# Kernel optimization log

Measured on AMD Instinct MI355X. Metric: run time of the kernel, lower is better.

Reference implementation:

```python
import jax, jax.numpy as jnp
import numpy as np

B, NV, NQ, NA = 128, 100, 14, 10
V_DIM, Q_DIM, A_DIM = 2048, 1024, 1024
H_DIM, RANK, HD, G = 512, 32, 16, 2  # HD = H_DIM // RANK, G = glimpse


def setup_inputs() -> dict:
    key = jax.random.key(0)
    ks = jax.random.split(key, 16)
    s = 0.05
    return {
        "v": jax.random.normal(ks[0], (B, NV, V_DIM), jnp.float32),
        "q": jax.random.normal(ks[1], (B, NQ, Q_DIM), jnp.float32),
        "a": jax.random.normal(ks[2], (B, NA, A_DIM), jnp.float32),
        # tucker projections (FCNet = Linear + ReLU; dropout identity at eval)
        "Wv": jax.random.normal(ks[3], (H_DIM, V_DIM), jnp.float32) * s,
        "bv": jnp.zeros((H_DIM,), jnp.float32),
        "Wq": jax.random.normal(ks[4], (H_DIM, Q_DIM), jnp.float32) * s,
        "bq": jnp.zeros((H_DIM,), jnp.float32),
        "Wa": jax.random.normal(ks[5], (H_DIM, A_DIM), jnp.float32) * s,
        "ba": jnp.zeros((H_DIM,), jnp.float32),
        # rank-wise projection nets, stacked over rank: [rank, HD, H_DIM]
        "Wvr": jax.random.normal(ks[6], (RANK, HD, H_DIM), jnp.float32) * s,
        "bvr": jnp.zeros((RANK, HD), jnp.float32),
        "Wqr": jax.random.normal(ks[7], (RANK, HD, H_DIM), jnp.float32) * s,
        "bqr": jnp.zeros((RANK, HD), jnp.float32),
        "War": jax.random.normal(ks[8], (RANK, HD, H_DIM), jnp.float32) * s,
        "bar": jnp.zeros((RANK, HD), jnp.float32),
        # Tucker core T_g with h_out squeezed: [rank, hv, hq, ha, glimpse]
        "T": jax.random.normal(ks[9], (RANK, HD, HD, HD, G), jnp.float32),
    }


def reference(v, q, a, Wv, bv, Wq, bq, Wa, ba, Wvr, bvr, Wqr, bqr, War, bar, T):
    relu = jax.nn.relu
    # modality tucker projections: [B, N, H_DIM]
    vt = relu(jnp.einsum('bnd,hd->bnh', v, Wv) + bv)
    qt = relu(jnp.einsum('bnd,hd->bnh', q, Wq) + bq)
    at = relu(jnp.einsum('bnd,hd->bnh', a, Wa) + ba)
    # rank-wise FCNets, batched over rank: [B, rank, N, HD]
    v_ = relu(jnp.einsum('bnh,rch->brnc', vt, Wvr) + bvr[None, :, None, :])
    q_ = relu(jnp.einsum('bnh,rch->brnc', qt, Wqr) + bqr[None, :, None, :])
    a_ = relu(jnp.einsum('bnh,rch->brnc', at, War) + bar[None, :, None, :])
    # 6-way Tucker contraction, summed over rank: [B, NV, NQ, NA, G]
    f_emb = jnp.einsum('rijkg,bnvi,bnqj,bnak->bvqag', T, v_, q_, a_,
                       optimize=True)
    return f_emb
```

## Files before the change

kernel.cpp:

```cpp
#include <hip/hip_runtime.h>
#include <cstddef>
#include <cstdint>

#define B_    128
#define NV_   100
#define NQ_   14
#define NA_   10
#define HDIM  512
#define RANK_ 32
#define HD_   16
#define G_    2

typedef __bf16 bf16x8 __attribute__((ext_vector_type(8)));
typedef float  f32x4  __attribute__((ext_vector_type(4)));
union Frag { uint4 u; bf16x8 v; };

__device__ __forceinline__ unsigned int f2bf(float f) {
  unsigned int u = __float_as_uint(f);
  u = (u + 0x7FFFu + ((u >> 16) & 1u)) >> 16;
  return u & 0xFFFFu;
}

__device__ __forceinline__ void gload_lds16(const unsigned short* gp,
                                            unsigned short* dp) {
  __builtin_amdgcn_global_load_lds(
      (const __attribute__((address_space(1))) void*)gp,
      (__attribute__((address_space(3))) void*)dp, 16, 0, 0);
}

__global__ __launch_bounds__(256) void cvt_kernel(
    const float* __restrict__ s0, const float* __restrict__ s1,
    const float* __restrict__ s2, const float* __restrict__ s3,
    const float* __restrict__ s4, const float* __restrict__ s5,
    const float* __restrict__ s6, const float* __restrict__ s7,
    unsigned short* __restrict__ dst)
{
  const int pref[8] = {896, 1536, 2048, 2304, 2560, 2688, 2816, 2944};
  const float* srcs[8] = {s0, s1, s2, s3, s4, s5, s6, s7};
  const int blk = blockIdx.x;
  int seg = 0;
  #pragma unroll
  for (int i = 0; i < 7; ++i) if (blk >= pref[i]) seg = i + 1;
  const int base_chunk = seg ? pref[seg - 1] : 0;
  const size_t loc = (size_t)(blk - base_chunk) * 2048 + threadIdx.x * 8;
  const float* s = srcs[seg] + loc;
  float4 f0 = *(const float4*)s;
  float4 f1 = *(const float4*)(s + 4);
  ushort4 o0, o1;
  o0.x = f2bf(f0.x); o0.y = f2bf(f0.y); o0.z = f2bf(f0.z); o0.w = f2bf(f0.w);
  o1.x = f2bf(f1.x); o1.y = f2bf(f1.y); o1.z = f2bf(f1.z); o1.w = f2bf(f1.w);
  unsigned short* d = dst + (size_t)blk * 2048 + threadIdx.x * 8;
  *(ushort4*)d = o0;
  *(ushort4*)(d + 4) = o1;
}

__device__ __forceinline__ void stage_swz8(const unsigned short* __restrict__ src,
                                           int K, unsigned short* dst, int t)
{
  const int wb = t & 448;
  const int l = t & 63;
  #pragma unroll
  for (int i = 0; i < 2; ++i) {
    const int sb = i * 512 + wb;
    const int li = sb + l;
    const int row = li >> 3;
    const int p = li & 7;
    const int s = p ^ (row & 7);
    gload_lds16(src + (size_t)row * K + s * 8, dst + sb * 8);
  }
}

__device__ __forceinline__ void cvt_write(const float4 f[4], unsigned short* Abuf,
                                          int ar, int kq)
{
  unsigned short* base = Abuf + ar * 64;
  #pragma unroll
  for (int j = 0; j < 2; ++j) {
    uint4 p;
    p.x = f2bf(f[2*j].x)   | (f2bf(f[2*j].y)   << 16);
    p.y = f2bf(f[2*j].z)   | (f2bf(f[2*j].w)   << 16);
    p.z = f2bf(f[2*j+1].x) | (f2bf(f[2*j+1].y) << 16);
    p.w = f2bf(f[2*j+1].z) | (f2bf(f[2*j+1].w) << 16);
    const int s = (kq * 2 + j) ^ (ar & 7);
    *(uint4*)&base[s * 8] = p;
  }
}

__global__ __launch_bounds__(512, 4) void l1_gemm(
    const float* __restrict__ v,
    const unsigned short* __restrict__ qb, const unsigned short* __restrict__ ab,
    const unsigned short* __restrict__ Wvb, const unsigned short* __restrict__ Wqb,
    const unsigned short* __restrict__ Wab,
    const float* __restrict__ bv, const float* __restrict__ bq,
    const float* __restrict__ ba,
    unsigned short* __restrict__ vtb, unsigned short* __restrict__ qtb,
    unsigned short* __restrict__ atb)
{
  __shared__ __align__(16) unsigned short As[2][8192];
  __shared__ __align__(16) unsigned short Bs[2][8192];
  const int bx = blockIdx.x;
  int grp, gx, gy, K;
  const unsigned short *A16 = qb, *W;
  const float* bias;
  unsigned short* C;
  if (bx < 400) {
    grp = 0; const int xcd = bx & 7, j = bx >> 3; const int m = xcd * 50 + j;
    gy = m >> 2; gx = m & 3; W = Wvb; bias = bv; C = vtb; K = 2048;
  } else if (bx < 456) {
    grp = 1; const int lo = bx - 400; gy = lo >> 2; gx = lo & 3;
    A16 = qb; W = Wqb; bias = bq; C = qtb; K = 1024;
  } else {
    grp = 2; const int lo = bx - 456; gy = lo >> 2; gx = lo & 3;
    A16 = ab; W = Wab; bias = ba; C = atb; K = 1024;
  }
  const int nsteps = K >> 6;
  const int bm = gy * 128, bn = gx * 128;
  const int t = threadIdx.x;
  const int w = t >> 6, l = t & 63;
  const int wm = (w >> 2) * 64, wn = (w & 3) * 32;

  f32x4 acc[4][2];
  #pragma unroll
  for (int i = 0; i < 4; ++i)
    #pragma unroll
    for (int j = 0; j < 2; ++j) acc[i][j] = f32x4{0.f, 0.f, 0.f, 0.f};

  const int ar = t >> 2, kq = t & 3;
  const float* vrow = (grp == 0)
      ? v + (size_t)(bm + ar) * 2048 + kq * 16 : (const float*)nullptr;
  float4 R0[4], R1[4];

  stage_swz8(W + (size_t)bn * K, K, Bs[0], t);
  if (grp == 0) {
    #pragma unroll
    for (int i = 0; i < 4; ++i) R0[i] = ((const float4*)vrow)[i];
    #pragma unroll
    for (int i = 0; i < 4; ++i) R1[i] = ((const float4*)(vrow + 64))[i];
    cvt_write(R0, As[0], ar, kq);
  } else {
    stage_swz8(A16 + (size_t)bm * K, K, As[0], t);
  }
  __syncthreads();

  for (int step = 0; step < nsteps; ++step) {
    const int db = step & 1;
    const bool hn = (step + 1) < nsteps;
    if (hn) stage_swz8(W + (size_t)bn * K + (step + 1) * 64, K, Bs[db ^ 1], t);
    if (grp == 0) {
      if (step + 2 < nsteps) {
        const float* p = vrow + (step + 2) * 64;
        if (db == 0) {
          #pragma unroll
          for (int i = 0; i < 4; ++i) R0[i] = ((const float4*)p)[i];
        } else {
          #pragma unroll
          for (int i = 0; i < 4; ++i) R1[i] = ((const float4*)p)[i];
        }
      }
      if (hn) {
        if (db == 0) cvt_write(R1, As[1], ar, kq);
        else         cvt_write(R0, As[0], ar, kq);
      }
    } else if (hn) {
      stage_swz8(A16 + (size_t)bm * K + (step + 1) * 64, K, As[db ^ 1], t);
    }
    const unsigned short* Ad = As[db];
    const unsigned short* Bd = Bs[db];
    #pragma unroll
    for (int ks = 0; ks < 2; ++ks) {
      Frag fa[4], fb[2];
      #pragma unroll
      for (int i = 0; i < 4; ++i) {
        const int r = wm + 16 * i + (l & 15);
        fa[i].u = *(const uint4*)&Ad[r * 64 + (((ks * 4 + (l >> 4)) ^ (r & 7)) * 8)];
      }
      #pragma unroll
      for (int j = 0; j < 2; ++j) {
        const int r = wn + 16 * j + (l & 15);
        fb[j].u = *(const uint4*)&Bd[r * 64 + (((ks * 4 + (l >> 4)) ^ (r & 7)) * 8)];
      }
      #pragma unroll
      for (int i = 0; i < 4; ++i)
        #pragma unroll
        for (int j = 0; j < 2; ++j)
          acc[i][j] = __builtin_amdgcn_mfma_f32_16x16x32_bf16(fa[i].v, fb[j].v, acc[i][j], 0, 0, 0);
    }
    __syncthreads();
  }

  const int q4 = (l >> 4) * 4, cl = l & 15;
  #pragma unroll
  for (int i = 0; i < 4; ++i)
    #pragma unroll
    for (int j = 0; j < 2; ++j) {
      const int col = bn + wn + 16 * j + cl;
      const float bs = bias[col];
      #pragma unroll
      for (int r = 0; r < 4; ++r) {
        const int row = bm + wm + 16 * i + q4 + r;
        float o = fmaxf(acc[i][j][r] + bs, 0.f);
        C[(size_t)row * 512 + col] = (unsigned short)f2bf(o);
      }
    }
}

__global__ __launch_bounds__(512, 4) void l2_gemm(
    const unsigned short* __restrict__ vtb, const unsigned short* __restrict__ qtb,
    const unsigned short* __restrict__ atb,
    const unsigned short* __restrict__ Wvrb, const unsigned short* __restrict__ Wqrb,
    const unsigned short* __restrict__ Warb,
    const float* __restrict__ bvr, const float* __restrict__ bqr,
    const float* __restrict__ bar,
    unsigned short* __restrict__ vrb, float* __restrict__ q_r, float* __restrict__ a_r)
{
  __shared__ __align__(16) unsigned short As[2][8192];
  __shared__ __align__(16) unsigned short Bs[2][8192];
  const int bx = blockIdx.x;
  int grp, gx, gy;
  const unsigned short *A16, *W;
  const float* bias;
  if (bx < 400) {
    grp = 0; const int xcd = bx & 7, j = bx >> 3; const int m = xcd * 50 + j;
    gy = m >> 2; gx = m & 3; A16 = vtb; W = Wvrb; bias = bvr;
  } else if (bx < 456) {
    grp = 1; const int lo = bx - 400; gy = lo >> 2; gx = lo & 3;
    A16 = qtb; W = Wqrb; bias = bqr;
  } else {
    grp = 2; const int lo = bx - 456; gy = lo >> 2; gx = lo & 3;
    A16 = atb; W = Warb; bias = bar;
  }
  const int bm = gy * 128, bn = gx * 128;
  const int t = threadIdx.x;
  const int w = t >> 6, l = t & 63;
  const int wm = (w >> 2) * 64, wn = (w & 3) * 32;

  f32x4 acc[4][2];
  #pragma unroll
  for (int i = 0; i < 4; ++i)
    #pragma unroll
    for (int j = 0; j < 2; ++j) acc[i][j] = f32x4{0.f, 0.f, 0.f, 0.f};

  stage_swz8(W + (size_t)bn * 512, 512, Bs[0], t);
  stage_swz8(A16 + (size_t)bm * 512, 512, As[0], t);
  __syncthreads();

  for (int step = 0; step < 8; ++step) {
    const int db = step & 1;
    const bool hn = (step + 1) < 8;
    const int k0n = (step + 1) << 6;
    if (hn) {
      stage_swz8(W + (size_t)bn * 512 + k0n, 512, Bs[db ^ 1], t);
      stage_swz8(A16 + (size_t)bm * 512 + k0n, 512, As[db ^ 1], t);
    }
    const unsigned short* Ad = As[db];
    const unsigned short* Bd = Bs[db];
    #pragma unroll
    for (int ks = 0; ks < 2; ++ks) {
      Frag fa[4], fb[2];
      #pragma unroll
      for (int i = 0; i < 4; ++i) {
        const int r = wm + 16 * i + (l & 15);
        fa[i].u = *(const uint4*)&Ad[r * 64 + (((ks * 4 + (l >> 4)) ^ (r & 7)) * 8)];
      }
      #pragma unroll
      for (int j = 0; j < 2; ++j) {
        const int r = wn + 16 * j + (l & 15);
        fb[j].u = *(const uint4*)&Bd[r * 64 + (((ks * 4 + (l >> 4)) ^ (r & 7)) * 8)];
      }
      #pragma unroll
      for (int i = 0; i < 4; ++i)
        #pragma unroll
        for (int j = 0; j < 2; ++j)
          acc[i][j] = __builtin_amdgcn_mfma_f32_16x16x32_bf16(fa[i].v, fb[j].v, acc[i][j], 0, 0, 0);
    }
    __syncthreads();
  }

  const int q4 = (l >> 4) * 4, cl = l & 15;
  #pragma unroll
  for (int i = 0; i < 4; ++i)
    #pragma unroll
    for (int j = 0; j < 2; ++j) {
      const int col = bn + wn + 16 * j + cl;
      const float bs = bias[col];
      #pragma unroll
      for (int r = 0; r < 4; ++r) {
        const int row = bm + wm + 16 * i + q4 + r;
        float o = fmaxf(acc[i][j][r] + bs, 0.f);
        if (grp == 0)      vrb[(size_t)row * 512 + col] = (unsigned short)f2bf(o);
        else if (grp == 1) q_r[(size_t)row * 512 + col] = o;
        else               a_r[(size_t)row * 512 + col] = o;
      }
    }
}

__global__ void tsum_kernel(const float* __restrict__ T, float* __restrict__ Tsum)
{
  const int idx = blockIdx.x * 256 + threadIdx.x;
  float s = 0.f;
  #pragma unroll
  for (int r = 0; r < RANK_; ++r) s += T[r * 8192 + idx];
  Tsum[idx] = s;
}

__global__ __launch_bounds__(256) void build_w_kernel(
    const float* __restrict__ q_, const float* __restrict__ a_,
    const float* __restrict__ Tsum, unsigned short* __restrict__ WmatT)
{
  const int n = blockIdx.x, b = blockIdx.y, t = threadIdx.x;
  __shared__ float Ts[8192];
  __shared__ float U[14 * 544];

  #pragma unroll
  for (int s = 0; s < 8; ++s)
    ((float4*)Ts)[s * 256 + t] = ((const float4*)Tsum)[s * 256 + t];
  __syncthreads();

  {
    const int i = t >> 4, k = t & 15;
    float acc0[NQ_], acc1[NQ_];
    #pragma unroll
    for (int q = 0; q < NQ_; ++q) { acc0[q] = 0.f; acc1[q] = 0.f; }
    const float* qbase = q_ + (size_t)b * NQ_ * HDIM + n * 16;
    #pragma unroll
    for (int j = 0; j < 16; ++j) {
      float2 ts = *(const float2*)&Ts[i * 512 + j * 32 + k * 2];
      #pragma unroll
      for (int q = 0; q < NQ_; ++q) {
        float qv = qbase[q * HDIM + j];
        acc0[q] += ts.x * qv;
        acc1[q] += ts.y * qv;
      }
    }
    #pragma unroll
    for (int q = 0; q < NQ_; ++q) {
      float2 uu; uu.x = acc0[q]; uu.y = acc1[q];
      *(float2*)&U[q * 544 + i * 34 + k * 2] = uu;
    }
  }
  __syncthreads();

  if ((t >> 4) < NQ_) {
    const int q = t >> 4, i = t & 15;
    float acc0[NA_], acc1[NA_];
    #pragma unroll
    for (int a = 0; a < NA_; ++a) { acc0[a] = 0.f; acc1[a] = 0.f; }
    const float* abase = a_ + (size_t)b * NA_ * HDIM + n * 16;
    #pragma unroll
    for (int k = 0; k < 16; ++k) {
      float2 uu = *(const float2*)&U[q * 544 + i * 34 + k * 2];
      #pragma unroll
      for (int a = 0; a < NA_; ++a) {
        float av = abase[a * HDIM + k];
        acc0[a] += uu.x * av;
        acc1[a] += uu.y * av;
      }
    }
    unsigned short* wb = WmatT + (size_t)b * 320 * 512 + (n * 16 + i);
    #pragma unroll
    for (int a = 0; a < NA_; ++a) {
      wb[(size_t)((q * 10 + a) * 2 + 0) * 512] = (unsigned short)f2bf(acc0[a]);
      wb[(size_t)((q * 10 + a) * 2 + 1) * 512] = (unsigned short)f2bf(acc1[a]);
    }
  }
}

__device__ __forceinline__ void final_stage(
    const unsigned short* __restrict__ Vrb, const unsigned short* __restrict__ Wb,
    int b, int mh, int n0, int k0, int t,
    unsigned short* Asb, unsigned short* Bsb)
{
  const int w = t >> 6, l = t & 63;
  {
    int grow = b * NV_ + mh * 64 + w * 16 + (l >> 2);
    if (grow > B_ * NV_ - 1) grow = B_ * NV_ - 1;
    gload_lds16(Vrb + (size_t)grow * HDIM + k0 + (l & 3) * 8, &Asb[w * 512]);
  }
  #pragma unroll
  for (int c = 0; c < 3; ++c) {
    const int base = c * 256 + w * 64;
    if (base < 640) {
      const int li = base + l;
      const int nrow = li >> 2, ko2 = (li & 3) * 8;
      gload_lds16(Wb + (size_t)(n0 + nrow) * 512 + k0 + ko2, &Bsb[base * 8]);
    }
  }
}

__global__ __launch_bounds__(256) void final_mfma(
    const unsigned short* __restrict__ Vrb, const unsigned short* __restrict__ WmatT,
    float* __restrict__ out)
{
  __shared__ __align__(16) unsigned short As[2][2048];
  __shared__ __align__(16) unsigned short Bs[2][5120];
  const int b  = blockIdx.y;
  const int mh = blockIdx.x >> 1;
  const int n0 = (blockIdx.x & 1) * 160;
  const int t = threadIdx.x;
  const int w = t >> 6, l = t & 63;
  const int wm = (w >> 1) * 32;
  const int wn = (w & 1) * 80;

  f32x4 acc[2][5];
  #pragma unroll
  for (int mi = 0; mi < 2; ++mi)
    #pragma unroll
    for (int nj = 0; nj < 5; ++nj) acc[mi][nj] = f32x4{0.f, 0.f, 0.f, 0.f};

  const unsigned short* Wb = WmatT + (size_t)b * 320 * 512;

  final_stage(Vrb, Wb, b, mh, n0, 0, t, As[0], Bs[0]);
  __syncthreads();

  for (int step = 0; step < 16; ++step) {
    const int db = step & 1;
    if (step + 1 < 16)
      final_stage(Vrb, Wb, b, mh, n0, (step + 1) * 32, t, As[db ^ 1], Bs[db ^ 1]);

    Frag fa[2], fb[5];
    #pragma unroll
    for (int mi = 0; mi < 2; ++mi)
      fa[mi].u = *(const uint4*)&As[db][(wm + mi * 16 + (l & 15)) * 32 + (l >> 4) * 8];
    #pragma unroll
    for (int nj = 0; nj < 5; ++nj)
      fb[nj].u = *(const uint4*)&Bs[db][(wn + nj * 16 + (l & 15)) * 32 + (l >> 4) * 8];
    #pragma unroll
    for (int mi = 0; mi < 2; ++mi)
      #pragma unroll
      for (int nj = 0; nj < 5; ++nj)
        acc[mi][nj] = __builtin_amdgcn_mfma_f32_16x16x32_bf16(fa[mi].v, fb[nj].v, acc[mi][nj], 0, 0, 0);
    __syncthreads();
  }

  #pragma unroll
  for (int mi = 0; mi < 2; ++mi)
    #pragma unroll
    for (int nj = 0; nj < 5; ++nj) {
      const int col = n0 + wn + nj * 16 + (l & 15);
      if (col < 280) {
        #pragma unroll
        for (int r = 0; r < 4; ++r) {
          const int row = mh * 64 + wm + mi * 16 + (l >> 4) * 4 + r;
          if (row < NV_)
            out[((size_t)b * NV_ + row) * 280 + col] = acc[mi][nj][r];
        }
      }
    }
}

extern "C" void kernel_launch(void* const* d_in, const int* in_sizes, int n_in,
                              void* d_out, int out_size, void* d_ws, size_t ws_size,
                              hipStream_t stream)
{
  const float* v   = (const float*)d_in[0];
  const float* q   = (const float*)d_in[1];
  const float* a   = (const float*)d_in[2];
  const float* Wv  = (const float*)d_in[3];
  const float* bv  = (const float*)d_in[4];
  const float* Wq  = (const float*)d_in[5];
  const float* bq  = (const float*)d_in[6];
  const float* Wa  = (const float*)d_in[7];
  const float* ba  = (const float*)d_in[8];
  const float* Wvr = (const float*)d_in[9];
  const float* bvr = (const float*)d_in[10];
  const float* Wqr = (const float*)d_in[11];
  const float* bqr = (const float*)d_in[12];
  const float* War = (const float*)d_in[13];
  const float* bar = (const float*)d_in[14];
  const float* T   = (const float*)d_in[15];

  unsigned short* wsu = (unsigned short*)d_ws;
  float* wsf = (float*)d_ws;

  unsigned short* WmatT = wsu;
  unsigned short* qb    = wsu;
  unsigned short* ab    = wsu + 1835008;
  unsigned short* Wvb   = wsu + 3145728;
  unsigned short* Wqb   = wsu + 4194304;
  unsigned short* Wab   = wsu + 4718592;
  unsigned short* Wvrb  = wsu + 5242880;
  unsigned short* Wqrb  = wsu + 5505024;
  unsigned short* Warb  = wsu + 5767168;
  unsigned short* vtb   = wsu + 20971520;
  unsigned short* qtb   = wsu + 27525120;
  unsigned short* atb   = wsu + 28442624;
  unsigned short* vrb   = wsu + 29097984;
  float* q_r  = wsf + 17825792;
  float* a_r  = wsf + 18743296;
  float* Tsum = wsf + 19398656;

  cvt_kernel<<<2944, 256, 0, stream>>>(q, a, Wv, Wq, Wa, Wvr, Wqr, War, wsu);

  l1_gemm<<<496, 512, 0, stream>>>(v, qb, ab, Wvb, Wqb, Wab, bv, bq, ba,
                                   vtb, qtb, atb);
  l2_gemm<<<496, 512, 0, stream>>>(vtb, qtb, atb, Wvrb, Wqrb, Warb,
                                   bvr, bqr, bar, vrb, q_r, a_r);

  tsum_kernel<<<32, 256, 0, stream>>>(T, Tsum);
  build_w_kernel<<<dim3(32, 128), 256, 0, stream>>>(q_r, a_r, Tsum, WmatT);
  final_mfma<<<dim3(4, 128), 256, 0, stream>>>(vrb, WmatT, (float*)d_out);
}
```

Before: 328.0 us.

## Deepen GEMM pipelines with triple-buffered weights and partial vmcnt barriers

Both projection GEMMs now keep two K-steps of loads in flight. Weight tiles go into a three-slot LDS ring, and activation tiles are staged through registers and written with swizzled LDS stores. The __syncthreads calls are replaced by custom barriers that wait only until vmcnt drops to 6, 4 or 0, so the latest prefetches stay outstanding across the barrier. This is meant to hide global latency better, at the cost of more LDS per block (occupancy risk) and fragile hand-tuned waitcnt correctness.

```diff
diff --git a/kernel.cpp b/kernel.cpp
--- a/kernel.cpp
+++ b/kernel.cpp
@@ -26,6 +26,22 @@
   __builtin_amdgcn_global_load_lds(
       (const __attribute__((address_space(1))) void*)gp,
       (__attribute__((address_space(3))) void*)dp, 16, 0, 0);
+}
+
+__device__ __forceinline__ void bar6() {
+  asm volatile("s_waitcnt vmcnt(6) expcnt(0) lgkmcnt(0)" ::: "memory");
+  __builtin_amdgcn_s_barrier();
+  asm volatile("" ::: "memory");
+}
+__device__ __forceinline__ void bar4() {
+  asm volatile("s_waitcnt vmcnt(4) expcnt(0) lgkmcnt(0)" ::: "memory");
+  __builtin_amdgcn_s_barrier();
+  asm volatile("" ::: "memory");
+}
+__device__ __forceinline__ void bar0() {
+  asm volatile("s_waitcnt vmcnt(0) expcnt(0) lgkmcnt(0)" ::: "memory");
+  __builtin_amdgcn_s_barrier();
+  asm volatile("" ::: "memory");
 }
 
 __global__ __launch_bounds__(256) void cvt_kernel(
@@ -70,19 +86,55 @@
   }
 }
 
-__device__ __forceinline__ void cvt_write(const float4 f[4], unsigned short* Abuf,
-                                          int ar, int kq)
+__device__ __forceinline__ void cvt_write(const float4 f0, const float4 f1,
+                                          const float4 f2, const float4 f3,
+                                          unsigned short* Abuf, int ar, int kq)
 {
   unsigned short* base = Abuf + ar * 64;
-  #pragma unroll
-  for (int j = 0; j < 2; ++j) {
-    uint4 p;
-    p.x = f2bf(f[2*j].x)   | (f2bf(f[2*j].y)   << 16);
-    p.y = f2bf(f[2*j].z)   | (f2bf(f[2*j].w)   << 16);
-    p.z = f2bf(f[2*j+1].x) | (f2bf(f[2*j+1].y) << 16);
-    p.w = f2bf(f[2*j+1].z) | (f2bf(f[2*j+1].w) << 16);
-    const int s = (kq * 2 + j) ^ (ar & 7);
-    *(uint4*)&base[s * 8] = p;
+  uint4 p0, p1;
+  p0.x = f2bf(f0.x) | (f2bf(f0.y) << 16);
+  p0.y = f2bf(f0.z) | (f2bf(f0.w) << 16);
+  p0.z = f2bf(f1.x) | (f2bf(f1.y) << 16);
+  p0.w = f2bf(f1.z) | (f2bf(f1.w) << 16);
+  p1.x = f2bf(f2.x) | (f2bf(f2.y) << 16);
+  p1.y = f2bf(f2.z) | (f2bf(f2.w) << 16);
+  p1.z = f2bf(f3.x) | (f2bf(f3.y) << 16);
+  p1.w = f2bf(f3.z) | (f2bf(f3.w) << 16);
+  *(uint4*)&base[((kq * 2 + 0) ^ (ar & 7)) * 8] = p0;
+  *(uint4*)&base[((kq * 2 + 1) ^ (ar & 7)) * 8] = p1;
+}
+
+__device__ __forceinline__ void bwrite(const uint4 u0, const uint4 u1,
+                                       unsigned short* Abuf, int ar, int kq)
+{
+  unsigned short* base = Abuf + ar * 64;
+  *(uint4*)&base[((kq * 2 + 0) ^ (ar & 7)) * 8] = u0;
+  *(uint4*)&base[((kq * 2 + 1) ^ (ar & 7)) * 8] = u1;
+}
+
+__device__ __forceinline__ void compute64(const unsigned short* Ad,
+                                          const unsigned short* Bd,
+                                          int wm, int wn, int l,
+                                          f32x4 acc[4][2])
+{
+  #pragma unroll
+  for (int ks = 0; ks < 2; ++ks) {
+    Frag fa[4], fb[2];
+    #pragma unroll
+    for (int i = 0; i < 4; ++i) {
+      const int r = wm + 16 * i + (l & 15);
+      fa[i].u = *(const uint4*)&Ad[r * 64 + (((ks * 4 + (l >> 4)) ^ (r & 7)) * 8)];
+    }
+    #pragma unroll
+    for (int j = 0; j < 2; ++j) {
+      const int r = wn + 16 * j + (l & 15);
+      fb[j].u = *(const uint4*)&Bd[r * 64 + (((ks * 4 + (l >> 4)) ^ (r & 7)) * 8)];
+    }
+    #pragma unroll
+    for (int i = 0; i < 4; ++i)
+      #pragma unroll
+      for (int j = 0; j < 2; ++j)
+        acc[i][j] = __builtin_amdgcn_mfma_f32_16x16x32_bf16(fa[i].v, fb[j].v, acc[i][j], 0, 0, 0);
   }
 }
 
@@ -97,7 +149,7 @@
     unsigned short* __restrict__ atb)
 {
   __shared__ __align__(16) unsigned short As[2][8192];
-  __shared__ __align__(16) unsigned short Bs[2][8192];
+  __shared__ __align__(16) unsigned short Bs[3][8192];
   const int bx = blockIdx.x;
   int grp, gx, gy, K;
   const unsigned short *A16 = qb, *W;
@@ -114,10 +166,18 @@
     A16 = ab; W = Wab; bias = ba; C = atb; K = 1024;
   }
   const int nsteps = K >> 6;
+  const bool isv = (grp == 0);
   const int bm = gy * 128, bn = gx * 128;
   const int t = threadIdx.x;
   const int w = t >> 6, l = t & 63;
   const int wm = (w >> 2) * 64, wn = (w & 3) * 32;
+  const int ar = t >> 2, kq = t & 3;
+
+  const float* vrow = isv ? v + (size_t)(bm + ar) * 2048 + kq * 16
+                          : (const float*)nullptr;
+  const unsigned short* arow = isv ? (const unsigned short*)nullptr
+                                   : A16 + (size_t)(bm + ar) * K + kq * 16;
+  const unsigned short* Wrow = W + (size_t)bn * K;
 
   f32x4 acc[4][2];
   #pragma unroll
@@ -125,67 +185,75 @@
     #pragma unroll
     for (int j = 0; j < 2; ++j) acc[i][j] = f32x4{0.f, 0.f, 0.f, 0.f};
 
-  const int ar = t >> 2, kq = t & 3;
-  const float* vrow = (grp == 0)
-      ? v + (size_t)(bm + ar) * 2048 + kq * 16 : (const float*)nullptr;
-  float4 R0[4], R1[4];
-
-  stage_swz8(W + (size_t)bn * K, K, Bs[0], t);
-  if (grp == 0) {
-    #pragma unroll
-    for (int i = 0; i < 4; ++i) R0[i] = ((const float4*)vrow)[i];
-    #pragma unroll
-    for (int i = 0; i < 4; ++i) R1[i] = ((const float4*)(vrow + 64))[i];
-    cvt_write(R0, As[0], ar, kq);
+  float4 RA0, RA1, RA2, RA3, RB0, RB1, RB2, RB3;
+  uint4 UA0, UA1, UB0, UB1;
+
+  if (isv) {
+    { const float4* p = (const float4*)vrow;
+      RA0 = p[0]; RA1 = p[1]; RA2 = p[2]; RA3 = p[3]; }
+    stage_swz8(Wrow, K, Bs[0], t);
+    { const float4* p = (const float4*)(vrow + 64);
+      RB0 = p[0]; RB1 = p[1]; RB2 = p[2]; RB3 = p[3]; }
+    stage_swz8(Wrow + 64, K, Bs[1], t);
+    cvt_write(RA0, RA1, RA2, RA3, As[0], ar, kq);
+    bar6();
   } else {
-    stage_swz8(A16 + (size_t)bm * K, K, As[0], t);
-  }
-  __syncthreads();
-
-  for (int step = 0; step < nsteps; ++step) {
-    const int db = step & 1;
-    const bool hn = (step + 1) < nsteps;
-    if (hn) stage_swz8(W + (size_t)bn * K + (step + 1) * 64, K, Bs[db ^ 1], t);
-    if (grp == 0) {
-      if (step + 2 < nsteps) {
-        const float* p = vrow + (step + 2) * 64;
-        if (db == 0) {
-          #pragma unroll
-          for (int i = 0; i < 4; ++i) R0[i] = ((const float4*)p)[i];
-        } else {
-          #pragma unroll
-          for (int i = 0; i < 4; ++i) R1[i] = ((const float4*)p)[i];
+    { const uint4* p = (const uint4*)arow; UA0 = p[0]; UA1 = p[1]; }
+    stage_swz8(Wrow, K, Bs[0], t);
+    { const uint4* p = (const uint4*)(arow + 64); UB0 = p[0]; UB1 = p[1]; }
+    stage_swz8(Wrow + 64, K, Bs[1], t);
+    bwrite(UA0, UA1, As[0], ar, kq);
+    bar4();
+  }
+
+  int bc = 0;
+  for (int kk = 0; kk < nsteps; kk += 2) {
+    {
+      const bool h2 = (kk + 2) < nsteps;
+      const int b2 = (bc == 0) ? 2 : bc - 1;
+      if (isv) {
+        if (h2) {
+          const float4* p = (const float4*)(vrow + (kk + 2) * 64);
+          RA0 = p[0]; RA1 = p[1]; RA2 = p[2]; RA3 = p[3];
+          stage_swz8(Wrow + (kk + 2) * 64, K, Bs[b2], t);
         }
-      }
-      if (hn) {
-        if (db == 0) cvt_write(R1, As[1], ar, kq);
-        else         cvt_write(R0, As[0], ar, kq);
-      }
-    } else if (hn) {
-      stage_swz8(A16 + (size_t)bm * K + (step + 1) * 64, K, As[db ^ 1], t);
-    }
-    const unsigned short* Ad = As[db];
-    const unsigned short* Bd = Bs[db];
-    #pragma unroll
-    for (int ks = 0; ks < 2; ++ks) {
-      Frag fa[4], fb[2];
-      #pragma unroll
-      for (int i = 0; i < 4; ++i) {
-        const int r = wm + 16 * i + (l & 15);
-        fa[i].u = *(const uint4*)&Ad[r * 64 + (((ks * 4 + (l >> 4)) ^ (r & 7)) * 8)];
-      }
-      #pragma unroll
-      for (int j = 0; j < 2; ++j) {
-        const int r = wn + 16 * j + (l & 15);
-        fb[j].u = *(const uint4*)&Bd[r * 64 + (((ks * 4 + (l >> 4)) ^ (r & 7)) * 8)];
-      }
-      #pragma unroll
-      for (int i = 0; i < 4; ++i)
-        #pragma unroll
-        for (int j = 0; j < 2; ++j)
-          acc[i][j] = __builtin_amdgcn_mfma_f32_16x16x32_bf16(fa[i].v, fb[j].v, acc[i][j], 0, 0, 0);
-    }
-    __syncthreads();
+        cvt_write(RB0, RB1, RB2, RB3, As[1], ar, kq);
+      } else {
+        if (h2) {
+          const uint4* p = (const uint4*)(arow + (kk + 2) * 64);
+          UA0 = p[0]; UA1 = p[1];
+          stage_swz8(Wrow + (kk + 2) * 64, K, Bs[b2], t);
+        }
+        bwrite(UB0, UB1, As[1], ar, kq);
+      }
+      compute64(As[0], Bs[bc], wm, wn, l, acc);
+      if (h2) { if (isv) bar6(); else bar4(); } else bar0();
+      bc = (bc == 2) ? 0 : bc + 1;
+    }
+    {
+      const int k1 = kk + 1;
+      const bool h2 = (k1 + 2) < nsteps;
+      const bool h1 = (k1 + 1) < nsteps;
+      const int b2 = (bc == 0) ? 2 : bc - 1;
+      if (isv) {
+        if (h2) {
+          const float4* p = (const float4*)(vrow + (k1 + 2) * 64);
+          RB0 = p[0]; RB1 = p[1]; RB2 = p[2]; RB3 = p[3];
+          stage_swz8(Wrow + (k1 + 2) * 64, K, Bs[b2], t);
+        }
+        if (h1) cvt_write(RA0, RA1, RA2, RA3, As[0], ar, kq);
+      } else {
+        if (h2) {
+          const uint4* p = (const uint4*)(arow + (k1 + 2) * 64);
+          UB0 = p[0]; UB1 = p[1];
+          stage_swz8(Wrow + (k1 + 2) * 64, K, Bs[b2], t);
+        }
+        if (h1) bwrite(UA0, UA1, As[0], ar, kq);
+      }
+      compute64(As[1], Bs[bc], wm, wn, l, acc);
+      if (h2) { if (isv) bar6(); else bar4(); } else bar0();
+      bc = (bc == 2) ? 0 : bc + 1;
+    }
   }
 
   const int q4 = (l >> 4) * 4, cl = l & 15;
@@ -210,11 +278,11 @@
     const unsigned short* __restrict__ Wvrb, const unsigned short* __restrict__ Wqrb,
     const unsigned short* __restrict__ Warb,
     const float* __restrict__ bvr, const float* __restrict__ bqr,
-    const float* __restrict__ bar,
+    const float* __restrict__ bar_,
     unsigned short* __restrict__ vrb, float* __restrict__ q_r, float* __restrict__ a_r)
 {
   __shared__ __align__(16) unsigned short As[2][8192];
-  __shared__ __align__(16) unsigned short Bs[2][8192];
+  __shared__ __align__(16) unsigned short Bs[3][8192];
   const int bx = blockIdx.x;
   int grp, gx, gy;
   const unsigned short *A16, *W;
@@ -227,12 +295,17 @@
     A16 = qtb; W = Wqrb; bias = bqr;
   } else {
     grp = 2; const int lo = bx - 456; gy = lo >> 2; gx = lo & 3;
-    A16 = atb; W = Warb; bias = bar;
-  }
+    A16 = atb; W = Warb; bias = bar_;
+  }
+  const int nsteps = 8;
   const int bm = gy * 128, bn = gx * 128;
   const int t = threadIdx.x;
   const int w = t >> 6, l = t & 63;
   const int wm = (w >> 2) * 64, wn = (w & 3) * 32;
+  const int ar = t >> 2, kq = t & 3;
+
+  const unsigned short* arow = A16 + (size_t)(bm + ar) * 512 + kq * 16;
+  const unsigned short* Wrow = W + (size_t)bn * 512;
 
   f32x4 acc[4][2];
   #pragma unroll
@@ -240,40 +313,45 @@
     #pragma unroll
     for (int j = 0; j < 2; ++j) acc[i][j] = f32x4{0.f, 0.f, 0.f, 0.f};
 
-  stage_swz8(W + (size_t)bn * 512, 512, Bs[0], t);
-  stage_swz8(A16 + (size_t)bm * 512, 512, As[0], t);
-  __syncthreads();
-
-  for (int step = 0; step < 8; ++step) {
-    const int db = step & 1;
-    const bool hn = (step + 1) < 8;
-    const int k0n = (step + 1) << 6;
-    if (hn) {
-      stage_swz8(W + (size_t)bn * 512 + k0n, 512, Bs[db ^ 1], t);
-      stage_swz8(A16 + (size_t)bm * 512 + k0n, 512, As[db ^ 1], t);
-    }
-    const unsigned short* Ad = As[db];
-    const unsigned short* Bd = Bs[db];
-    #pragma unroll
-    for (int ks = 0; ks < 2; ++ks) {
-      Frag fa[4], fb[2];
-      #pragma unroll
-      for (int i = 0; i < 4; ++i) {
-        const int r = wm + 16 * i + (l & 15);
-        fa[i].u = *(const uint4*)&Ad[r * 64 + (((ks * 4 + (l >> 4)) ^ (r & 7)) * 8)];
-      }
-      #pragma unroll
-      for (int j = 0; j < 2; ++j) {
-        const int r = wn + 16 * j + (l & 15);
-        fb[j].u = *(const uint4*)&Bd[r * 64 + (((ks * 4 + (l >> 4)) ^ (r & 7)) * 8)];
-      }
-      #pragma unroll
-      for (int i = 0; i < 4; ++i)
-        #pragma unroll
-        for (int j = 0; j < 2; ++j)
-          acc[i][j] = __builtin_amdgcn_mfma_f32_16x16x32_bf16(fa[i].v, fb[j].v, acc[i][j], 0, 0, 0);
-    }
-    __syncthreads();
+  uint4 UA0, UA1, UB0, UB1;
+
+  { const uint4* p = (const uint4*)arow; UA0 = p[0]; UA1 = p[1]; }
+  stage_swz8(Wrow, 512, Bs[0], t);
+  { const uint4* p = (const uint4*)(arow + 64); UB0 = p[0]; UB1 = p[1]; }
+  stage_swz8(Wrow + 64, 512, Bs[1], t);
+  bwrite(UA0, UA1, As[0], ar, kq);
+  bar4();
+
+  int bc = 0;
+  for (int kk = 0; kk < nsteps; kk += 2) {
+    {
+      const bool h2 = (kk + 2) < nsteps;
+      const int b2 = (bc == 0) ? 2 : bc - 1;
+      if (h2) {
+        const uint4* p = (const uint4*)(arow + (kk + 2) * 64);
+        UA0 = p[0]; UA1 = p[1];
+        stage_swz8(Wrow + (kk + 2) * 64, 512, Bs[b2], t);
+      }
+      bwrite(UB0, UB1, As[1], ar, kq);
+      compute64(As[0], Bs[bc], wm, wn, l, acc);
+      if (h2) bar4(); else bar0();
+      bc = (bc == 2) ? 0 : bc + 1;
+    }
+    {
+      const int k1 = kk + 1;
+      const bool h2 = (k1 + 2) < nsteps;
+      const bool h1 = (k1 + 1) < nsteps;
+      const int b2 = (bc == 0) ? 2 : bc - 1;
+      if (h2) {
+        const uint4* p = (const uint4*)(arow + (k1 + 2) * 64);
+        UB0 = p[0]; UB1 = p[1];
+        stage_swz8(Wrow + (k1 + 2) * 64, 512, Bs[b2], t);
+      }
+      if (h1) bwrite(UA0, UA1, As[0], ar, kq);
+      compute64(As[1], Bs[bc], wm, wn, l, acc);
+      if (h2) bar4(); else bar0();
+      bc = (bc == 2) ? 0 : bc + 1;
+    }
   }
 
   const int q4 = (l >> 4) * 4, cl = l & 15;
```

New measurement: 342.2 us. 4.3% more time.

## Split K across warp halves with 64x64 warp tiles and LDS reduction

Applied to the files above, without the earlier changes.

Both GEMM kernels now give each wave a 64x64 output tile over one half of each 64-wide K slice, so each pair of waves splits K. The partial sums are combined through shared memory after the main loop. The goal is better fragment reuse: more MFMAs per LDS fragment load. The cost is double the accumulator registers, which may lower occupancy at launch bounds (512,4), plus an extra LDS reduction pass and barrier.

```diff
diff --git a/kernel.cpp b/kernel.cpp
--- a/kernel.cpp
+++ b/kernel.cpp
@@ -70,20 +70,46 @@
   }
 }
 
-__device__ __forceinline__ void cvt_write(const float4 f[4], unsigned short* Abuf,
-                                          int ar, int kq)
+__device__ __forceinline__ void cvt_write(const float4 f0, const float4 f1,
+                                          const float4 f2, const float4 f3,
+                                          unsigned short* Abuf, int ar, int kq)
 {
   unsigned short* base = Abuf + ar * 64;
-  #pragma unroll
-  for (int j = 0; j < 2; ++j) {
-    uint4 p;
-    p.x = f2bf(f[2*j].x)   | (f2bf(f[2*j].y)   << 16);
-    p.y = f2bf(f[2*j].z)   | (f2bf(f[2*j].w)   << 16);
-    p.z = f2bf(f[2*j+1].x) | (f2bf(f[2*j+1].y) << 16);
-    p.w = f2bf(f[2*j+1].z) | (f2bf(f[2*j+1].w) << 16);
-    const int s = (kq * 2 + j) ^ (ar & 7);
-    *(uint4*)&base[s * 8] = p;
-  }
+  uint4 p0, p1;
+  p0.x = f2bf(f0.x) | (f2bf(f0.y) << 16);
+  p0.y = f2bf(f0.z) | (f2bf(f0.w) << 16);
+  p0.z = f2bf(f1.x) | (f2bf(f1.y) << 16);
+  p0.w = f2bf(f1.z) | (f2bf(f1.w) << 16);
+  p1.x = f2bf(f2.x) | (f2bf(f2.y) << 16);
+  p1.y = f2bf(f2.z) | (f2bf(f2.w) << 16);
+  p1.z = f2bf(f3.x) | (f2bf(f3.y) << 16);
+  p1.w = f2bf(f3.z) | (f2bf(f3.w) << 16);
+  *(uint4*)&base[((kq * 2 + 0) ^ (ar & 7)) * 8] = p0;
+  *(uint4*)&base[((kq * 2 + 1) ^ (ar & 7)) * 8] = p1;
+}
+
+__device__ __forceinline__ void compute_h(const unsigned short* Ad,
+                                          const unsigned short* Bd,
+                                          int wm, int wn, int kh, int l,
+                                          f32x4 acc[4][4])
+{
+  Frag fa[4], fb[4];
+  const int slot = kh * 4 + (l >> 4);
+  #pragma unroll
+  for (int i = 0; i < 4; ++i) {
+    const int r = wm + 16 * i + (l & 15);
+    fa[i].u = *(const uint4*)&Ad[r * 64 + ((slot ^ (r & 7)) * 8)];
+  }
+  #pragma unroll
+  for (int j = 0; j < 4; ++j) {
+    const int r = wn + 16 * j + (l & 15);
+    fb[j].u = *(const uint4*)&Bd[r * 64 + ((slot ^ (r & 7)) * 8)];
+  }
+  #pragma unroll
+  for (int i = 0; i < 4; ++i)
+    #pragma unroll
+    for (int j = 0; j < 4; ++j)
+      acc[i][j] = __builtin_amdgcn_mfma_f32_16x16x32_bf16(fa[i].v, fb[j].v, acc[i][j], 0, 0, 0);
 }
 
 __global__ __launch_bounds__(512, 4) void l1_gemm(
@@ -96,8 +122,9 @@
     unsigned short* __restrict__ vtb, unsigned short* __restrict__ qtb,
     unsigned short* __restrict__ atb)
 {
-  __shared__ __align__(16) unsigned short As[2][8192];
-  __shared__ __align__(16) unsigned short Bs[2][8192];
+  __shared__ __align__(16) unsigned short SH[32768];
+  unsigned short (*As)[8192] = (unsigned short (*)[8192])(SH);
+  unsigned short (*Bs)[8192] = (unsigned short (*)[8192])(SH + 16384);
   const int bx = blockIdx.x;
   int grp, gx, gy, K;
   const unsigned short *A16 = qb, *W;
@@ -114,29 +141,31 @@
     A16 = ab; W = Wab; bias = ba; C = atb; K = 1024;
   }
   const int nsteps = K >> 6;
+  const bool isv = (grp == 0);
   const int bm = gy * 128, bn = gx * 128;
   const int t = threadIdx.x;
   const int w = t >> 6, l = t & 63;
-  const int wm = (w >> 2) * 64, wn = (w & 3) * 32;
-
-  f32x4 acc[4][2];
+  const int qd = w & 3, kh = w >> 2;
+  const int wm = (qd >> 1) * 64, wn = (qd & 1) * 64;
+  const int ar = t >> 2, kq = t & 3;
+
+  f32x4 acc[4][4];
   #pragma unroll
   for (int i = 0; i < 4; ++i)
     #pragma unroll
-    for (int j = 0; j < 2; ++j) acc[i][j] = f32x4{0.f, 0.f, 0.f, 0.f};
-
-  const int ar = t >> 2, kq = t & 3;
-  const float* vrow = (grp == 0)
-      ? v + (size_t)(bm + ar) * 2048 + kq * 16 : (const float*)nullptr;
-  float4 R0[4], R1[4];
+    for (int j = 0; j < 4; ++j) acc[i][j] = f32x4{0.f, 0.f, 0.f, 0.f};
+
+  const float* vrow = isv ? v + (size_t)(bm + ar) * 2048 + kq * 16
+                          : (const float*)nullptr;
+  float4 R0, R1, R2, R3, R4, R5, R6, R7;
 
   stage_swz8(W + (size_t)bn * K, K, Bs[0], t);
-  if (grp == 0) {
-    #pragma unroll
-    for (int i = 0; i < 4; ++i) R0[i] = ((const float4*)vrow)[i];
-    #pragma unroll
-    for (int i = 0; i < 4; ++i) R1[i] = ((const float4*)(vrow + 64))[i];
-    cvt_write(R0, As[0], ar, kq);
+  if (isv) {
+    { const float4* p = (const float4*)vrow;
+      R0 = p[0]; R1 = p[1]; R2 = p[2]; R3 = p[3]; }
+    { const float4* p = (const float4*)(vrow + 64);
+      R4 = p[0]; R5 = p[1]; R6 = p[2]; R7 = p[3]; }
+    cvt_write(R0, R1, R2, R3, As[0], ar, kq);
   } else {
     stage_swz8(A16 + (size_t)bm * K, K, As[0], t);
   }
@@ -146,59 +175,64 @@
     const int db = step & 1;
     const bool hn = (step + 1) < nsteps;
     if (hn) stage_swz8(W + (size_t)bn * K + (step + 1) * 64, K, Bs[db ^ 1], t);
-    if (grp == 0) {
+    if (isv) {
       if (step + 2 < nsteps) {
         const float* p = vrow + (step + 2) * 64;
         if (db == 0) {
-          #pragma unroll
-          for (int i = 0; i < 4; ++i) R0[i] = ((const float4*)p)[i];
+          const float4* q4p = (const float4*)p;
+          R0 = q4p[0]; R1 = q4p[1]; R2 = q4p[2]; R3 = q4p[3];
         } else {
-          #pragma unroll
-          for (int i = 0; i < 4; ++i) R1[i] = ((const float4*)p)[i];
+          const float4* q4p = (const float4*)p;
+          R4 = q4p[0]; R5 = q4p[1]; R6 = q4p[2]; R7 = q4p[3];
         }
       }
       if (hn) {
-        if (db == 0) cvt_write(R1, As[1], ar, kq);
-        else         cvt_write(R0, As[0], ar, kq);
+        if (db == 0) cvt_write(R4, R5, R6, R7, As[1], ar, kq);
+        else         cvt_write(R0, R1, R2, R3, As[0], ar, kq);
       }
     } else if (hn) {
       stage_swz8(A16 + (size_t)bm * K + (step + 1) * 64, K, As[db ^ 1], t);
     }
-    const unsigned short* Ad = As[db];
-    const unsigned short* Bd = Bs[db];
-    #pragma unroll
-    for (int ks = 0; ks < 2; ++ks) {
-      Frag fa[4], fb[2];
-      #pragma unroll
-      for (int i = 0; i < 4; ++i) {
-        const int r = wm + 16 * i + (l & 15);
-        fa[i].u = *(const uint4*)&Ad[r * 64 + (((ks * 4 + (l >> 4)) ^ (r & 7)) * 8)];
-      }
-      #pragma unroll
-      for (int j = 0; j < 2; ++j) {
-        const int r = wn + 16 * j + (l & 15);
-        fb[j].u = *(const uint4*)&Bd[r * 64 + (((ks * 4 + (l >> 4)) ^ (r & 7)) * 8)];
-      }
-      #pragma unroll
-      for (int i = 0; i < 4; ++i)
+    compute_h(As[db], Bs[db], wm, wn, kh, l, acc);
+    __syncthreads();
+  }
+
+  float* red = (float*)SH;
+  const int q4 = (l >> 4) * 4, cl = l & 15;
+  {
+    float* dst = red + (kh ? 0 : 8192) + qd * 2048;
+    const int ig = kh ? 0 : 2;
+    #pragma unroll
+    for (int ii = 0; ii < 2; ++ii)
+      #pragma unroll
+      for (int j = 0; j < 4; ++j)
         #pragma unroll
-        for (int j = 0; j < 2; ++j)
-          acc[i][j] = __builtin_amdgcn_mfma_f32_16x16x32_bf16(fa[i].v, fb[j].v, acc[i][j], 0, 0, 0);
-    }
-    __syncthreads();
-  }
-
-  const int q4 = (l >> 4) * 4, cl = l & 15;
-  #pragma unroll
-  for (int i = 0; i < 4; ++i)
-    #pragma unroll
-    for (int j = 0; j < 2; ++j) {
+        for (int r = 0; r < 4; ++r)
+          dst[(ii * 16 + q4 + r) * 64 + 16 * j + cl] = acc[ig + ii][j][r];
+  }
+  __syncthreads();
+  const int ik = kh ? 2 : 0;
+  {
+    const float* src = red + (kh ? 8192 : 0) + qd * 2048;
+    #pragma unroll
+    for (int ii = 0; ii < 2; ++ii)
+      #pragma unroll
+      for (int j = 0; j < 4; ++j)
+        #pragma unroll
+        for (int r = 0; r < 4; ++r)
+          acc[ik + ii][j][r] += src[(ii * 16 + q4 + r) * 64 + 16 * j + cl];
+  }
+
+  #pragma unroll
+  for (int ii = 0; ii < 2; ++ii)
+    #pragma unroll
+    for (int j = 0; j < 4; ++j) {
       const int col = bn + wn + 16 * j + cl;
       const float bs = bias[col];
       #pragma unroll
       for (int r = 0; r < 4; ++r) {
-        const int row = bm + wm + 16 * i + q4 + r;
-        float o = fmaxf(acc[i][j][r] + bs, 0.f);
+        const int row = bm + wm + 16 * (ik + ii) + q4 + r;
+        float o = fmaxf(acc[ik + ii][j][r] + bs, 0.f);
         C[(size_t)row * 512 + col] = (unsigned short)f2bf(o);
       }
     }
@@ -210,11 +244,12 @@
     const unsigned short* __restrict__ Wvrb, const unsigned short* __restrict__ Wqrb,
     const unsigned short* __restrict__ Warb,
     const float* __restrict__ bvr, const float* __restrict__ bqr,
-    const float* __restrict__ bar,
+    const float* __restrict__ bar_,
     unsigned short* __restrict__ vrb, float* __restrict__ q_r, float* __restrict__ a_r)
 {
-  __shared__ __align__(16) unsigned short As[2][8192];
-  __shared__ __align__(16) unsigned short Bs[2][8192];
+  __shared__ __align__(16) unsigned short SH[32768];
+  unsigned short (*As)[8192] = (unsigned short (*)[8192])(SH);
+  unsigned short (*Bs)[8192] = (unsigned short (*)[8192])(SH + 16384);
   const int bx = blockIdx.x;
   int grp, gx, gy;
   const unsigned short *A16, *W;
@@ -227,66 +262,73 @@
     A16 = qtb; W = Wqrb; bias = bqr;
   } else {
     grp = 2; const int lo = bx - 456; gy = lo >> 2; gx = lo & 3;
-    A16 = atb; W = Warb; bias = bar;
-  }
+    A16 = atb; W = Warb; bias = bar_;
+  }
+  const int nsteps = 8;
   const int bm = gy * 128, bn = gx * 128;
   const int t = threadIdx.x;
   const int w = t >> 6, l = t & 63;
-  const int wm = (w >> 2) * 64, wn = (w & 3) * 32;
-
-  f32x4 acc[4][2];
+  const int qd = w & 3, kh = w >> 2;
+  const int wm = (qd >> 1) * 64, wn = (qd & 1) * 64;
+
+  f32x4 acc[4][4];
   #pragma unroll
   for (int i = 0; i < 4; ++i)
     #pragma unroll
-    for (int j = 0; j < 2; ++j) acc[i][j] = f32x4{0.f, 0.f, 0.f, 0.f};
+    for (int j = 0; j < 4; ++j) acc[i][j] = f32x4{0.f, 0.f, 0.f, 0.f};
 
   stage_swz8(W + (size_t)bn * 512, 512, Bs[0], t);
   stage_swz8(A16 + (size_t)bm * 512, 512, As[0], t);
   __syncthreads();
 
-  for (int step = 0; step < 8; ++step) {
+  for (int step = 0; step < nsteps; ++step) {
     const int db = step & 1;
-    const bool hn = (step + 1) < 8;
+    const bool hn = (step + 1) < nsteps;
     const int k0n = (step + 1) << 6;
     if (hn) {
       stage_swz8(W + (size_t)bn * 512 + k0n, 512, Bs[db ^ 1], t);
       stage_swz8(A16 + (size_t)bm * 512 + k0n, 512, As[db ^ 1], t);
     }
-    const unsigned short* Ad = As[db];
-    const unsigned short* Bd = Bs[db];
-    #pragma unroll
-    for (int ks = 0; ks < 2; ++ks) {
-      Frag fa[4], fb[2];
-      #pragma unroll
-      for (int i = 0; i < 4; ++i) {
-        const int r = wm + 16 * i + (l & 15);
-        fa[i].u = *(const uint4*)&Ad[r * 64 + (((ks * 4 + (l >> 4)) ^ (r & 7)) * 8)];
-      }
-      #pragma unroll
-      for (int j = 0; j < 2; ++j) {
-        const int r = wn + 16 * j + (l & 15);
-        fb[j].u = *(const uint4*)&Bd[r * 64 + (((ks * 4 + (l >> 4)) ^ (r & 7)) * 8)];
-      }
-      #pragma unroll
-      for (int i = 0; i < 4; ++i)
+    compute_h(As[db], Bs[db], wm, wn, kh, l, acc);
+    __syncthreads();
+  }
+
+  float* red = (float*)SH;
+  const int q4 = (l >> 4) * 4, cl = l & 15;
+  {
+    float* dst = red + (kh ? 0 : 8192) + qd * 2048;
+    const int ig = kh ? 0 : 2;
+    #pragma unroll
+    for (int ii = 0; ii < 2; ++ii)
+      #pragma unroll
+      for (int j = 0; j < 4; ++j)
         #pragma unroll
-        for (int j = 0; j < 2; ++j)
-          acc[i][j] = __builtin_amdgcn_mfma_f32_16x16x32_bf16(fa[i].v, fb[j].v, acc[i][j], 0, 0, 0);
-    }
-    __syncthreads();
-  }
-
-  const int q4 = (l >> 4) * 4, cl = l & 15;
-  #pragma unroll
-  for (int i = 0; i < 4; ++i)
-    #pragma unroll
-    for (int j = 0; j < 2; ++j) {
+        for (int r = 0; r < 4; ++r)
+          dst[(ii * 16 + q4 + r) * 64 + 16 * j + cl] = acc[ig + ii][j][r];
+  }
+  __syncthreads();
+  const int ik = kh ? 2 : 0;
+  {
+    const float* src = red + (kh ? 8192 : 0) + qd * 2048;
+    #pragma unroll
+    for (int ii = 0; ii < 2; ++ii)
+      #pragma unroll
+      for (int j = 0; j < 4; ++j)
+        #pragma unroll
+        for (int r = 0; r < 4; ++r)
+          acc[ik + ii][j][r] += src[(ii * 16 + q4 + r) * 64 + 16 * j + cl];
+  }
+
+  #pragma unroll
+  for (int ii = 0; ii < 2; ++ii)
+    #pragma unroll
+    for (int j = 0; j < 4; ++j) {
       const int col = bn + wn + 16 * j + cl;
       const float bs = bias[col];
       #pragma unroll
       for (int r = 0; r < 4; ++r) {
-        const int row = bm + wm + 16 * i + q4 + r;
-        float o = fmaxf(acc[i][j][r] + bs, 0.f);
+        const int row = bm + wm + 16 * (ik + ii) + q4 + r;
+        float o = fmaxf(acc[ik + ii][j][r] + bs, 0.f);
         if (grp == 0)      vrb[(size_t)row * 512 + col] = (unsigned short)f2bf(o);
         else if (grp == 1) q_r[(size_t)row * 512 + col] = o;
         else               a_r[(size_t)row * 512 + col] = o;
```

After: 1.135 ms. 246% more time.

## Single-buffer weight tiles in L1/L2 GEMMs to raise occupancy to 6 blocks

Applied to the files above, without the earlier changes.

Both projection GEMMs now keep the weight (B) tile in a single LDS buffer instead of a double buffer, cutting shared memory per block from 64KB to 48KB, and launch_bounds is raised from 4 to 6 blocks per CU. The weight tile for the current step is now loaded synchronously inside the loop with an extra barrier before compute, so B-tile loads are no longer overlapped with MFMA work. The intent is that higher occupancy hides that latency across blocks, but the tighter register limit could cause spills, and the extra per-step barrier adds stalls.

```diff
diff --git a/kernel.cpp b/kernel.cpp
--- a/kernel.cpp
+++ b/kernel.cpp
@@ -70,23 +70,51 @@
   }
 }
 
-__device__ __forceinline__ void cvt_write(const float4 f[4], unsigned short* Abuf,
-                                          int ar, int kq)
+__device__ __forceinline__ void cvt_write(const float4 f0, const float4 f1,
+                                          const float4 f2, const float4 f3,
+                                          unsigned short* Abuf, int ar, int kq)
 {
   unsigned short* base = Abuf + ar * 64;
-  #pragma unroll
-  for (int j = 0; j < 2; ++j) {
-    uint4 p;
-    p.x = f2bf(f[2*j].x)   | (f2bf(f[2*j].y)   << 16);
-    p.y = f2bf(f[2*j].z)   | (f2bf(f[2*j].w)   << 16);
-    p.z = f2bf(f[2*j+1].x) | (f2bf(f[2*j+1].y) << 16);
-    p.w = f2bf(f[2*j+1].z) | (f2bf(f[2*j+1].w) << 16);
-    const int s = (kq * 2 + j) ^ (ar & 7);
-    *(uint4*)&base[s * 8] = p;
-  }
-}
-
-__global__ __launch_bounds__(512, 4) void l1_gemm(
+  uint4 p0, p1;
+  p0.x = f2bf(f0.x) | (f2bf(f0.y) << 16);
+  p0.y = f2bf(f0.z) | (f2bf(f0.w) << 16);
+  p0.z = f2bf(f1.x) | (f2bf(f1.y) << 16);
+  p0.w = f2bf(f1.z) | (f2bf(f1.w) << 16);
+  p1.x = f2bf(f2.x) | (f2bf(f2.y) << 16);
+  p1.y = f2bf(f2.z) | (f2bf(f2.w) << 16);
+  p1.z = f2bf(f3.x) | (f2bf(f3.y) << 16);
+  p1.w = f2bf(f3.z) | (f2bf(f3.w) << 16);
+  *(uint4*)&base[((kq * 2 + 0) ^ (ar & 7)) * 8] = p0;
+  *(uint4*)&base[((kq * 2 + 1) ^ (ar & 7)) * 8] = p1;
+}
+
+__device__ __forceinline__ void compute64(const unsigned short* Ad,
+                                          const unsigned short* Bd,
+                                          int wm, int wn, int l,
+                                          f32x4 acc[4][2])
+{
+  #pragma unroll
+  for (int ks = 0; ks < 2; ++ks) {
+    Frag fa[4], fb[2];
+    #pragma unroll
+    for (int i = 0; i < 4; ++i) {
+      const int r = wm + 16 * i + (l & 15);
+      fa[i].u = *(const uint4*)&Ad[r * 64 + (((ks * 4 + (l >> 4)) ^ (r & 7)) * 8)];
+    }
+    #pragma unroll
+    for (int j = 0; j < 2; ++j) {
+      const int r = wn + 16 * j + (l & 15);
+      fb[j].u = *(const uint4*)&Bd[r * 64 + (((ks * 4 + (l >> 4)) ^ (r & 7)) * 8)];
+    }
+    #pragma unroll
+    for (int i = 0; i < 4; ++i)
+      #pragma unroll
+      for (int j = 0; j < 2; ++j)
+        acc[i][j] = __builtin_amdgcn_mfma_f32_16x16x32_bf16(fa[i].v, fb[j].v, acc[i][j], 0, 0, 0);
+  }
+}
+
+__global__ __launch_bounds__(512, 6) void l1_gemm(
     const float* __restrict__ v,
     const unsigned short* __restrict__ qb, const unsigned short* __restrict__ ab,
     const unsigned short* __restrict__ Wvb, const unsigned short* __restrict__ Wqb,
@@ -97,7 +125,7 @@
     unsigned short* __restrict__ atb)
 {
   __shared__ __align__(16) unsigned short As[2][8192];
-  __shared__ __align__(16) unsigned short Bs[2][8192];
+  __shared__ __align__(16) unsigned short Bs1[8192];
   const int bx = blockIdx.x;
   int grp, gx, gy, K;
   const unsigned short *A16 = qb, *W;
@@ -114,10 +142,16 @@
     A16 = ab; W = Wab; bias = ba; C = atb; K = 1024;
   }
   const int nsteps = K >> 6;
+  const bool isv = (grp == 0);
   const int bm = gy * 128, bn = gx * 128;
   const int t = threadIdx.x;
   const int w = t >> 6, l = t & 63;
   const int wm = (w >> 2) * 64, wn = (w & 3) * 32;
+  const int ar = t >> 2, kq = t & 3;
+
+  const float* vrow = isv ? v + (size_t)(bm + ar) * 2048 + kq * 16
+                          : (const float*)nullptr;
+  const unsigned short* Wrow = W + (size_t)bn * K;
 
   f32x4 acc[4][2];
   #pragma unroll
@@ -125,67 +159,38 @@
     #pragma unroll
     for (int j = 0; j < 2; ++j) acc[i][j] = f32x4{0.f, 0.f, 0.f, 0.f};
 
-  const int ar = t >> 2, kq = t & 3;
-  const float* vrow = (grp == 0)
-      ? v + (size_t)(bm + ar) * 2048 + kq * 16 : (const float*)nullptr;
-  float4 R0[4], R1[4];
-
-  stage_swz8(W + (size_t)bn * K, K, Bs[0], t);
-  if (grp == 0) {
-    #pragma unroll
-    for (int i = 0; i < 4; ++i) R0[i] = ((const float4*)vrow)[i];
-    #pragma unroll
-    for (int i = 0; i < 4; ++i) R1[i] = ((const float4*)(vrow + 64))[i];
-    cvt_write(R0, As[0], ar, kq);
+  float4 R0, R1, R2, R3, R4, R5, R6, R7;
+
+  if (isv) {
+    { const float4* p = (const float4*)vrow;
+      R0 = p[0]; R1 = p[1]; R2 = p[2]; R3 = p[3]; }
+    { const float4* p = (const float4*)(vrow + 64);
+      R4 = p[0]; R5 = p[1]; R6 = p[2]; R7 = p[3]; }
+    cvt_write(R0, R1, R2, R3, As[0], ar, kq);
   } else {
     stage_swz8(A16 + (size_t)bm * K, K, As[0], t);
   }
-  __syncthreads();
-
+
+  int db = 0;
   for (int step = 0; step < nsteps; ++step) {
-    const int db = step & 1;
-    const bool hn = (step + 1) < nsteps;
-    if (hn) stage_swz8(W + (size_t)bn * K + (step + 1) * 64, K, Bs[db ^ 1], t);
-    if (grp == 0) {
+    __syncthreads();
+    stage_swz8(Wrow + step * 64, K, Bs1, t);
+    if (isv && (step + 1) < nsteps) {
+      if ((step + 1) & 1) cvt_write(R4, R5, R6, R7, As[db ^ 1], ar, kq);
+      else                cvt_write(R0, R1, R2, R3, As[db ^ 1], ar, kq);
+    }
+    __syncthreads();
+    if (isv) {
       if (step + 2 < nsteps) {
-        const float* p = vrow + (step + 2) * 64;
-        if (db == 0) {
-          #pragma unroll
-          for (int i = 0; i < 4; ++i) R0[i] = ((const float4*)p)[i];
-        } else {
-          #pragma unroll
-          for (int i = 0; i < 4; ++i) R1[i] = ((const float4*)p)[i];
-        }
-      }
-      if (hn) {
-        if (db == 0) cvt_write(R1, As[1], ar, kq);
-        else         cvt_write(R0, As[0], ar, kq);
-      }
-    } else if (hn) {
+        const float4* p = (const float4*)(vrow + (step + 2) * 64);
+        if (step & 1) { R4 = p[0]; R5 = p[1]; R6 = p[2]; R7 = p[3]; }
+        else          { R0 = p[0]; R1 = p[1]; R2 = p[2]; R3 = p[3]; }
+      }
+    } else if (step + 1 < nsteps) {
       stage_swz8(A16 + (size_t)bm * K + (step + 1) * 64, K, As[db ^ 1], t);
     }
-    const unsigned short* Ad = As[db];
-    const unsigned short* Bd = Bs[db];
-    #pragma unroll
-    for (int ks = 0; ks < 2; ++ks) {
-      Frag fa[4], fb[2];
-      #pragma unroll
-      for (int i = 0; i < 4; ++i) {
-        const int r = wm + 16 * i + (l & 15);
-        fa[i].u = *(const uint4*)&Ad[r * 64 + (((ks * 4 + (l >> 4)) ^ (r & 7)) * 8)];
-      }
-      #pragma unroll
-      for (int j = 0; j < 2; ++j) {
-        const int r = wn + 16 * j + (l & 15);
-        fb[j].u = *(const uint4*)&Bd[r * 64 + (((ks * 4 + (l >> 4)) ^ (r & 7)) * 8)];
-      }
-      #pragma unroll
-      for (int i = 0; i < 4; ++i)
-        #pragma unroll
-        for (int j = 0; j < 2; ++j)
-          acc[i][j] = __builtin_amdgcn_mfma_f32_16x16x32_bf16(fa[i].v, fb[j].v, acc[i][j], 0, 0, 0);
-    }
-    __syncthreads();
+    compute64(As[db], Bs1, wm, wn, l, acc);
+    db ^= 1;
   }
 
   const int q4 = (l >> 4) * 4, cl = l & 15;
@@ -204,17 +209,17 @@
     }
 }
 
-__global__ __launch_bounds__(512, 4) void l2_gemm(
+__global__ __launch_bounds__(512, 6) void l2_gemm(
     const unsigned short* __restrict__ vtb, const unsigned short* __restrict__ qtb,
     const unsigned short* __restrict__ atb,
     const unsigned short* __restrict__ Wvrb, const unsigned short* __restrict__ Wqrb,
     const unsigned short* __restrict__ Warb,
     const float* __restrict__ bvr, const float* __restrict__ bqr,
-    const float* __restrict__ bar,
+    const float* __restrict__ bar_,
     unsigned short* __restrict__ vrb, float* __restrict__ q_r, float* __restrict__ a_r)
 {
   __shared__ __align__(16) unsigned short As[2][8192];
-  __shared__ __align__(16) unsigned short Bs[2][8192];
+  __shared__ __align__(16) unsigned short Bs1[8192];
   const int bx = blockIdx.x;
   int grp, gx, gy;
   const unsigned short *A16, *W;
@@ -227,12 +232,14 @@
     A16 = qtb; W = Wqrb; bias = bqr;
   } else {
     grp = 2; const int lo = bx - 456; gy = lo >> 2; gx = lo & 3;
-    A16 = atb; W = Warb; bias = bar;
-  }
+    A16 = atb; W = Warb; bias = bar_;
+  }
+  const int nsteps = 8;
   const int bm = gy * 128, bn = gx * 128;
   const int t = threadIdx.x;
   const int w = t >> 6, l = t & 63;
   const int wm = (w >> 2) * 64, wn = (w & 3) * 32;
+  const unsigned short* Wrow = W + (size_t)bn * 512;
 
   f32x4 acc[4][2];
   #pragma unroll
@@ -240,40 +247,17 @@
     #pragma unroll
     for (int j = 0; j < 2; ++j) acc[i][j] = f32x4{0.f, 0.f, 0.f, 0.f};
 
-  stage_swz8(W + (size_t)bn * 512, 512, Bs[0], t);
   stage_swz8(A16 + (size_t)bm * 512, 512, As[0], t);
-  __syncthreads();
-
-  for (int step = 0; step < 8; ++step) {
-    const int db = step & 1;
-    const bool hn = (step + 1) < 8;
-    const int k0n = (step + 1) << 6;
-    if (hn) {
-      stage_swz8(W + (size_t)bn * 512 + k0n, 512, Bs[db ^ 1], t);
-      stage_swz8(A16 + (size_t)bm * 512 + k0n, 512, As[db ^ 1], t);
-    }
-    const unsigned short* Ad = As[db];
-    const unsigned short* Bd = Bs[db];
-    #pragma unroll
-    for (int ks = 0; ks < 2; ++ks) {
-      Frag fa[4], fb[2];
-      #pragma unroll
-      for (int i = 0; i < 4; ++i) {
-        const int r = wm + 16 * i + (l & 15);
-        fa[i].u = *(const uint4*)&Ad[r * 64 + (((ks * 4 + (l >> 4)) ^ (r & 7)) * 8)];
-      }
-      #pragma unroll
-      for (int j = 0; j < 2; ++j) {
-        const int r = wn + 16 * j + (l & 15);
-        fb[j].u = *(const uint4*)&Bd[r * 64 + (((ks * 4 + (l >> 4)) ^ (r & 7)) * 8)];
-      }
-      #pragma unroll
-      for (int i = 0; i < 4; ++i)
-        #pragma unroll
-        for (int j = 0; j < 2; ++j)
-          acc[i][j] = __builtin_amdgcn_mfma_f32_16x16x32_bf16(fa[i].v, fb[j].v, acc[i][j], 0, 0, 0);
-    }
+
+  int db = 0;
+  for (int step = 0; step < nsteps; ++step) {
     __syncthreads();
+    stage_swz8(Wrow + step * 64, 512, Bs1, t);
+    __syncthreads();
+    if (step + 1 < nsteps)
+      stage_swz8(A16 + (size_t)bm * 512 + (step + 1) * 64, 512, As[db ^ 1], t);
+    compute64(As[db], Bs1, wm, wn, l, acc);
+    db ^= 1;
   }
 
   const int q4 = (l >> 4) * 4, cl = l & 15;
```

Measured after the change: 463.9 us. +41.4%, slower.
